# Performance work log

Measured on AMD Instinct MI355X. Metric: run time of the kernel, lower is better.

Reference implementation:

```python
import jax, jax.numpy as jnp
import numpy as np

B, S, D, V = 2, 2048, 4096, 32000

def setup_inputs() -> dict:
    key = jax.random.key(0)
    k1, k2, k3 = jax.random.split(key, 3)
    hidden_states = jax.random.normal(k1, (B, S, D), dtype=jnp.float32)
    W = jax.random.normal(k2, (V, D), dtype=jnp.float32) * 0.02  # lm_head weight [vocab, hidden]
    label_ids = jax.random.randint(k3, (B, S), 0, V, dtype=jnp.int64)
    return {"hidden_states": hidden_states, "W": W, "label_ids": label_ids}

def reference(hidden_states, W, label_ids):
    # lm_head: Linear(D, V, bias=False) -> logits [B, S, V], cast to fp32
    logits = jnp.einsum('bsd,vd->bsv', hidden_states, W).astype(jnp.float32)
    # shift: predict token t+1 from position t
    shift_logits = logits[:, :-1, :].reshape(-1, V)          # [B*(S-1), V]
    shift_labels = label_ids[:, 1:].reshape(-1)              # [B*(S-1)]
    logp = jax.nn.log_softmax(shift_logits, axis=-1)
    nll = -jnp.take_along_axis(logp, shift_labels[:, None], axis=1)[:, 0]
    loss = jnp.mean(nll)  # CrossEntropyLoss default reduction='mean'
    return loss, logits
```

## Files before the change

kernel.cpp:

```cpp
#include <hip/hip_runtime.h>
#include <hip/hip_bf16.h>

#define M_ 4096
#define N_ 32000
#define K_ 4096
#define S_ 2048
#define SM1 2047
#define NROWS 4094
#define NT_ 128

typedef __bf16 bf16x8 __attribute__((ext_vector_type(8)));
typedef float f32x4 __attribute__((ext_vector_type(4)));

#define GLDS16(g, l)                                                         \
  __builtin_amdgcn_global_load_lds(                                          \
      (__attribute__((address_space(1))) const void*)(g),                    \
      (__attribute__((address_space(3))) void*)(l), 16, 0, 0)
#define BAR() __builtin_amdgcn_s_barrier()
#define PRIO1() __builtin_amdgcn_s_setprio(1)
#define PRIO0() __builtin_amdgcn_s_setprio(0)
#define VMCNT(n) asm volatile("s_waitcnt vmcnt(" #n ")" ::: "memory")
#define LGKM0() asm volatile("s_waitcnt lgkmcnt(0)" ::: "memory")

__global__ __launch_bounds__(256) void cvt_f32_to_bf16(
    const float* __restrict__ in, bf16x8* __restrict__ out, long n8) {
  long i0 = (long)blockIdx.x * blockDim.x + threadIdx.x;
  long stride = (long)gridDim.x * blockDim.x;
  for (long i = i0; i < n8; i += stride) {
    const float4* p = reinterpret_cast<const float4*>(in) + i * 2;
    float4 a = p[0];
    float4 b = p[1];
    bf16x8 v;
    v[0] = (__bf16)a.x; v[1] = (__bf16)a.y; v[2] = (__bf16)a.z; v[3] = (__bf16)a.w;
    v[4] = (__bf16)b.x; v[5] = (__bf16)b.y; v[6] = (__bf16)b.z; v[7] = (__bf16)b.w;
    out[i] = v;
  }
}

__global__ __launch_bounds__(512, 2) void gemm256(
    const __bf16* __restrict__ A, const __bf16* __restrict__ B,
    float* __restrict__ C) {
  __shared__ __align__(1024) unsigned char smem[4][32768];

  const int tid = threadIdx.x;
  const int bid = blockIdx.x;
  const int wg = (bid & 7) * 250 + (bid >> 3);
  const int nblk = wg >> 4;
  const int mblk = wg & 15;
  const int m0 = mblk * 256;
  const int n0 = nblk * 256;

  const int w = tid >> 6;
  const int lane = tid & 63;
  const int wm = w >> 2;
  const int wn = w & 3;
  const int rl = lane & 15;
  const int cl = lane >> 4;

  f32x4 acc[8][4];
#pragma unroll
  for (int i = 0; i < 8; ++i)
#pragma unroll
    for (int j = 0; j < 4; ++j) acc[i][j] = (f32x4){0.f, 0.f, 0.f, 0.f};

  auto stA = [&](unsigned char* buf, int kt) {
#pragma unroll
    for (int j = 0; j < 2; ++j) {
      const int cd = j * 512 + tid;
      const int row = cd >> 2;
      const int c = (cd & 3) ^ (row & 3);
      GLDS16(A + (size_t)(m0 + row) * K_ + kt * 32 + c * 8, buf + cd * 16);
    }
  };
  auto stB = [&](unsigned char* buf, int kt) {
#pragma unroll
    for (int j = 0; j < 2; ++j) {
      const int cd = j * 512 + tid;
      const int row = cd >> 2;
      const int c = (cd & 3) ^ (row & 3);
      GLDS16(B + (size_t)(n0 + row) * K_ + kt * 32 + c * 8,
             buf + 16384 + cd * 16);
    }
  };
  auto ld = [&](const unsigned char* base, int row) -> bf16x8 {
    return *(const bf16x8*)(base + row * 64 + (((cl ^ row) & 3) << 4));
  };

  stA(smem[0], 0); stB(smem[0], 0);
  stA(smem[1], 1); stB(smem[1], 1);
  stA(smem[2], 2); stB(smem[2], 2);
  VMCNT(8);
  BAR();

  bf16x8 a[4], b[4];
  for (int s = 0; s < NT_; ++s) {
    const unsigned char* bufc = smem[s & 3];
    unsigned char* bufn = smem[(s + 3) & 3];
    const bool st = (s < NT_ - 3);

#pragma unroll
    for (int i = 0; i < 4; ++i) a[i] = ld(bufc, wm * 128 + i * 16 + rl);
#pragma unroll
    for (int j = 0; j < 4; ++j) b[j] = ld(bufc + 16384, wn * 64 + j * 16 + rl);
    if (st) stA(bufn, s + 3);
    BAR();
    LGKM0();
    PRIO1();
#pragma unroll
    for (int ii = 0; ii < 4; ++ii)
#pragma unroll
      for (int jj = 0; jj < 4; ++jj)
        acc[ii][jj] = __builtin_amdgcn_mfma_f32_16x16x32_bf16(
            a[ii], b[jj], acc[ii][jj], 0, 0, 0);
    PRIO0();
    BAR();

#pragma unroll
    for (int i = 0; i < 4; ++i) a[i] = ld(bufc, wm * 128 + 64 + i * 16 + rl);
    if (st) stB(bufn, s + 3);
    BAR();
    LGKM0();
    PRIO1();
#pragma unroll
    for (int ii = 0; ii < 4; ++ii)
#pragma unroll
      for (int jj = 0; jj < 4; ++jj)
        acc[4 + ii][jj] = __builtin_amdgcn_mfma_f32_16x16x32_bf16(
            a[ii], b[jj], acc[4 + ii][jj], 0, 0, 0);
    PRIO0();
    if (s < NT_ - 3) { VMCNT(8); }
    else if (s == NT_ - 3) { VMCNT(4); }
    else if (s == NT_ - 2) { VMCNT(0); }
    BAR();
  }

#pragma unroll
  for (int i = 0; i < 8; ++i)
#pragma unroll
    for (int j = 0; j < 4; ++j)
#pragma unroll
      for (int r = 0; r < 4; ++r) {
        const int grow = m0 + wm * 128 + i * 16 + cl * 4 + r;
        const int gcol = n0 + wn * 64 + j * 16 + rl;
        C[(size_t)grow * N_ + gcol] = acc[i][j][r];
      }
}

__global__ __launch_bounds__(256) void gemm_fb(const float* __restrict__ Ap,
                                               const float* __restrict__ Bp,
                                               float* __restrict__ Cp) {
  __shared__ __align__(1024) unsigned char smem[2][16384];
  const int tid = threadIdx.x;
  const int bid = blockIdx.x;
  const int swz = (bid & 7) * 1000 + (bid >> 3);
  const int nblk = swz >> 5;
  const int mblk = swz & 31;
  const int m0 = mblk * 128;
  const int n0 = nblk * 128;
  const int w = tid >> 6, lane = tid & 63;
  const int wm = w >> 1, wn = w & 1;
  const int rl = lane & 15, cl = lane >> 4;

  f32x4 acc[4][4];
#pragma unroll
  for (int i = 0; i < 4; ++i)
#pragma unroll
    for (int j = 0; j < 4; ++j) acc[i][j] = (f32x4){0.f, 0.f, 0.f, 0.f};

  auto stage = [&](int buf, int kt) {
    const int k0 = kt * 32;
#pragma unroll
    for (int j = 0; j < 2; ++j) {
      const int t = j * 256 + tid;
      const int row = t >> 2;
      const int c = t & 3;
      const int rp = row >> 1;
      const int pp = ((row & 1) * 4 + c) ^ (rp & 7);
      const int lb = rp * 128 + pp * 16;
      {
        const float4* g = (const float4*)(Ap + (size_t)(m0 + row) * K_ + k0 + c * 8);
        float4 x = g[0], y = g[1];
        bf16x8 v;
        v[0] = (__bf16)x.x; v[1] = (__bf16)x.y; v[2] = (__bf16)x.z; v[3] = (__bf16)x.w;
        v[4] = (__bf16)y.x; v[5] = (__bf16)y.y; v[6] = (__bf16)y.z; v[7] = (__bf16)y.w;
        *(bf16x8*)(&smem[buf][lb]) = v;
      }
      {
        const float4* g = (const float4*)(Bp + (size_t)(n0 + row) * K_ + k0 + c * 8);
        float4 x = g[0], y = g[1];
        bf16x8 v;
        v[0] = (__bf16)x.x; v[1] = (__bf16)x.y; v[2] = (__bf16)x.z; v[3] = (__bf16)x.w;
        v[4] = (__bf16)y.x; v[5] = (__bf16)y.y; v[6] = (__bf16)y.z; v[7] = (__bf16)y.w;
        *(bf16x8*)(&smem[buf][8192 + lb]) = v;
      }
    }
  };
  auto ldfrag = [&](const unsigned char* base, int row, int c) -> bf16x8 {
    const int rp = row >> 1;
    const int pp = ((row & 1) * 4 + c) ^ (rp & 7);
    return *(const bf16x8*)(base + rp * 128 + pp * 16);
  };
  auto compute = [&](int buf) {
    const unsigned char* bA = smem[buf];
    const unsigned char* bB = smem[buf] + 8192;
    bf16x8 af[4], bfv[4];
#pragma unroll
    for (int i = 0; i < 4; ++i) af[i] = ldfrag(bA, wm * 64 + i * 16 + rl, cl);
#pragma unroll
    for (int j = 0; j < 4; ++j) bfv[j] = ldfrag(bB, wn * 64 + j * 16 + rl, cl);
#pragma unroll
    for (int i = 0; i < 4; ++i)
#pragma unroll
      for (int j = 0; j < 4; ++j)
        acc[i][j] = __builtin_amdgcn_mfma_f32_16x16x32_bf16(af[i], bfv[j],
                                                            acc[i][j], 0, 0, 0);
  };

  stage(0, 0);
  __syncthreads();
  for (int kt = 0; kt < 128; kt += 2) {
    if (kt + 1 < 128) stage(1, kt + 1);
    compute(0);
    __syncthreads();
    if (kt + 2 < 128) stage(0, kt + 2);
    compute(1);
    __syncthreads();
  }
#pragma unroll
  for (int i = 0; i < 4; ++i)
#pragma unroll
    for (int j = 0; j < 4; ++j)
#pragma unroll
      for (int r = 0; r < 4; ++r) {
        const int grow = m0 + wm * 64 + i * 16 + cl * 4 + r;
        const int gcol = n0 + wn * 64 + j * 16 + rl;
        Cp[(size_t)grow * N_ + gcol] = acc[i][j][r];
      }
}

__global__ __launch_bounds__(256) void ce_rows(const float* __restrict__ logits,
                                               const int* __restrict__ labels,
                                               float* __restrict__ nll) {
  const int r = blockIdx.x;
  const int b = r / SM1;
  const int t = r - b * SM1;
  const float* row = logits + (size_t)(b * S_ + t) * N_;
  float m = -3.4e38f, s = 0.f;
  const float4* row4 = (const float4*)row;
  for (int i = threadIdx.x; i < 7936; i += 256) {
    float4 v = row4[i];
    float mx = fmaxf(fmaxf(v.x, v.y), fmaxf(v.z, v.w));
    if (mx > m) { s *= __expf(m - mx); m = mx; }
    s += __expf(v.x - m) + __expf(v.y - m) + __expf(v.z - m) + __expf(v.w - m);
  }
  {
    float v = row[31744 + threadIdx.x];
    if (v > m) { s *= __expf(m - v); m = v; }
    s += __expf(v - m);
  }
#pragma unroll
  for (int o = 32; o > 0; o >>= 1) {
    float m2 = __shfl_xor(m, o), s2 = __shfl_xor(s, o);
    float mn = fmaxf(m, m2);
    s = s * __expf(m - mn) + s2 * __expf(m2 - mn);
    m = mn;
  }
  __shared__ float rm[4], rs[4];
  if ((threadIdx.x & 63) == 0) { rm[threadIdx.x >> 6] = m; rs[threadIdx.x >> 6] = s; }
  __syncthreads();
  if (threadIdx.x == 0) {
    float M = fmaxf(fmaxf(rm[0], rm[1]), fmaxf(rm[2], rm[3]));
    float S = rs[0] * __expf(rm[0] - M) + rs[1] * __expf(rm[1] - M) +
              rs[2] * __expf(rm[2] - M) + rs[3] * __expf(rm[3] - M);
    nll[r] = M + __logf(S) - row[labels[b * S_ + t + 1]];
  }
}

__global__ __launch_bounds__(256) void reduce_loss(const float* __restrict__ nll,
                                                   float* __restrict__ out) {
  float s = 0.f;
  for (int i = threadIdx.x; i < NROWS; i += 256) s += nll[i];
#pragma unroll
  for (int o = 32; o > 0; o >>= 1) s += __shfl_xor(s, o);
  __shared__ float sb[4];
  if ((threadIdx.x & 63) == 0) sb[threadIdx.x >> 6] = s;
  __syncthreads();
  if (threadIdx.x == 0) out[0] = (sb[0] + sb[1] + sb[2] + sb[3]) / (float)NROWS;
}

extern "C" void kernel_launch(void* const* d_in, const int* in_sizes, int n_in,
                              void* d_out, int out_size, void* d_ws,
                              size_t ws_size, hipStream_t stream) {
  const float* h = (const float*)d_in[0];
  const float* Wf = (const float*)d_in[1];
  const int* labels = (const int*)d_in[2];
  float* out = (float*)d_out;
  float* logits = out + 1;

  const size_t abytes = (size_t)M_ * K_ * 2;
  const size_t bbytes = (size_t)N_ * K_ * 2;
  const size_t need = abytes + bbytes + (size_t)NROWS * sizeof(float);

  if (ws_size >= need) {
    unsigned char* base = (unsigned char*)d_ws;
    __bf16* hA = (__bf16*)base;
    __bf16* wB = (__bf16*)(base + abytes);
    float* nll = (float*)(base + abytes + bbytes);
    cvt_f32_to_bf16<<<2048, 256, 0, stream>>>(h, (bf16x8*)hA,
                                              (long)((size_t)M_ * K_ / 8));
    cvt_f32_to_bf16<<<4096, 256, 0, stream>>>(Wf, (bf16x8*)wB,
                                              (long)((size_t)N_ * K_ / 8));
    gemm256<<<2000, 512, 0, stream>>>(hA, wB, logits);
    ce_rows<<<4094, 256, 0, stream>>>(logits, labels, nll);
    reduce_loss<<<1, 256, 0, stream>>>(nll, out);
  } else {
    float* nll = (float*)d_ws;
    gemm_fb<<<8000, 256, 0, stream>>>(h, Wf, logits);
    ce_rows<<<4094, 256, 0, stream>>>(logits, labels, nll);
    reduce_loss<<<1, 256, 0, stream>>>(nll, out);
  }
}
```

Before: 1.351 ms.

## Restructure gemm256 main loop to BK=64 double-buffer with quartered MFMA phases

```diff
diff --git a/kernel.cpp b/kernel.cpp
--- a/kernel.cpp
+++ b/kernel.cpp
@@ -7,7 +7,7 @@
 #define S_ 2048
 #define SM1 2047
 #define NROWS 4094
-#define NT_ 128
+#define NT_ 64
 
 typedef __bf16 bf16x8 __attribute__((ext_vector_type(8)));
 typedef float f32x4 __attribute__((ext_vector_type(4)));
@@ -20,7 +20,6 @@
 #define PRIO1() __builtin_amdgcn_s_setprio(1)
 #define PRIO0() __builtin_amdgcn_s_setprio(0)
 #define VMCNT(n) asm volatile("s_waitcnt vmcnt(" #n ")" ::: "memory")
-#define LGKM0() asm volatile("s_waitcnt lgkmcnt(0)" ::: "memory")
 
 __global__ __launch_bounds__(256) void cvt_f32_to_bf16(
     const float* __restrict__ in, bf16x8* __restrict__ out, long n8) {
@@ -40,7 +39,7 @@
 __global__ __launch_bounds__(512, 2) void gemm256(
     const __bf16* __restrict__ A, const __bf16* __restrict__ B,
     float* __restrict__ C) {
-  __shared__ __align__(1024) unsigned char smem[4][32768];
+  __shared__ __align__(1024) unsigned char smem[2][65536];
 
   const int tid = threadIdx.x;
   const int bid = blockIdx.x;
@@ -56,6 +55,8 @@
   const int wn = w & 3;
   const int rl = lane & 15;
   const int cl = lane >> 4;
+  const int srow = tid >> 3;
+  const int scc = tid & 7;
 
   f32x4 acc[8][4];
 #pragma unroll
@@ -63,75 +64,132 @@
 #pragma unroll
     for (int j = 0; j < 4; ++j) acc[i][j] = (f32x4){0.f, 0.f, 0.f, 0.f};
 
-  auto stA = [&](unsigned char* buf, int kt) {
+  auto stA2 = [&](int nbuf, int kt, int q) {
 #pragma unroll
     for (int j = 0; j < 2; ++j) {
-      const int cd = j * 512 + tid;
-      const int row = cd >> 2;
-      const int c = (cd & 3) ^ (row & 3);
-      GLDS16(A + (size_t)(m0 + row) * K_ + kt * 32 + c * 8, buf + cd * 16);
+      const int r0 = q * 64 + j * 128;
+      const int row = r0 + srow;
+      const int c = scc ^ (row & 7);
+      GLDS16(A + (size_t)(m0 + row) * K_ + kt * 64 + c * 8,
+             &smem[nbuf][r0 * 128 + tid * 16]);
     }
   };
-  auto stB = [&](unsigned char* buf, int kt) {
+  auto stB2 = [&](int nbuf, int kt, int q) {
 #pragma unroll
     for (int j = 0; j < 2; ++j) {
-      const int cd = j * 512 + tid;
-      const int row = cd >> 2;
-      const int c = (cd & 3) ^ (row & 3);
-      GLDS16(B + (size_t)(n0 + row) * K_ + kt * 32 + c * 8,
-             buf + 16384 + cd * 16);
+      const int cg = j * 512 + tid;
+      const int rl_ = cg >> 3;
+      const int row = ((rl_ >> 5) << 6) + q * 32 + (rl_ & 31);
+      const int cc = cg & 7;
+      const int c = cc ^ (row & 7);
+      GLDS16(B + (size_t)(n0 + row) * K_ + kt * 64 + c * 8,
+             &smem[nbuf][32768 + row * 128 + cc * 16]);
     }
   };
-  auto ld = [&](const unsigned char* base, int row) -> bf16x8 {
-    return *(const bf16x8*)(base + row * 64 + (((cl ^ row) & 3) << 4));
-  };
-
-  stA(smem[0], 0); stB(smem[0], 0);
-  stA(smem[1], 1); stB(smem[1], 1);
-  stA(smem[2], 2); stB(smem[2], 2);
-  VMCNT(8);
+  auto ld = [&](const unsigned char* base, int row, int c) -> bf16x8 {
+    return *(const bf16x8*)(base + row * 128 + (((c ^ row) & 7) << 4));
+  };
+
+  stA2(0, 0, 0); stB2(0, 0, 0); stA2(0, 0, 1); stB2(0, 0, 1);
+  VMCNT(4);
   BAR();
 
-  bf16x8 a[4], b[4];
+  bf16x8 al[4][2], ah[4][2], b0r[2][2], b1r[2][2];
+#pragma unroll
+  for (int jj = 0; jj < 2; ++jj)
+#pragma unroll
+    for (int ks = 0; ks < 2; ++ks)
+      b0r[jj][ks] = ld(smem[0] + 32768, wn * 64 + jj * 16 + rl, ks * 4 + cl);
+#pragma unroll
+  for (int ii = 0; ii < 4; ++ii)
+#pragma unroll
+    for (int ks = 0; ks < 2; ++ks)
+      al[ii][ks] = ld(smem[0], wm * 128 + ii * 16 + rl, ks * 4 + cl);
+
   for (int s = 0; s < NT_; ++s) {
-    const unsigned char* bufc = smem[s & 3];
-    unsigned char* bufn = smem[(s + 3) & 3];
-    const bool st = (s < NT_ - 3);
-
-#pragma unroll
-    for (int i = 0; i < 4; ++i) a[i] = ld(bufc, wm * 128 + i * 16 + rl);
-#pragma unroll
-    for (int j = 0; j < 4; ++j) b[j] = ld(bufc + 16384, wn * 64 + j * 16 + rl);
-    if (st) stA(bufn, s + 3);
+    const int cur = s & 1;
+    const int nxt = cur ^ 1;
+    const unsigned char* bA = smem[cur];
+    const unsigned char* bB = smem[cur] + 32768;
+    const bool st = (s + 1 < NT_);
+
+    if (st) stA2(nxt, s + 1, 0);
+    PRIO1();
+#pragma unroll
+    for (int ii = 0; ii < 4; ++ii)
+#pragma unroll
+      for (int jj = 0; jj < 2; ++jj)
+#pragma unroll
+        for (int ks = 0; ks < 2; ++ks)
+          acc[ii][jj] = __builtin_amdgcn_mfma_f32_16x16x32_bf16(
+              al[ii][ks], b0r[jj][ks], acc[ii][jj], 0, 0, 0);
+    PRIO0();
+    if (st) { VMCNT(2); } else { VMCNT(0); }
     BAR();
-    LGKM0();
+
+    if (st) stB2(nxt, s + 1, 0);
+#pragma unroll
+    for (int jj = 0; jj < 2; ++jj)
+#pragma unroll
+      for (int ks = 0; ks < 2; ++ks)
+        b1r[jj][ks] = ld(bB, wn * 64 + 32 + jj * 16 + rl, ks * 4 + cl);
+#pragma unroll
+    for (int ii = 0; ii < 4; ++ii)
+#pragma unroll
+      for (int ks = 0; ks < 2; ++ks)
+        ah[ii][ks] = ld(bA, wm * 128 + 64 + ii * 16 + rl, ks * 4 + cl);
     PRIO1();
 #pragma unroll
     for (int ii = 0; ii < 4; ++ii)
 #pragma unroll
-      for (int jj = 0; jj < 4; ++jj)
-        acc[ii][jj] = __builtin_amdgcn_mfma_f32_16x16x32_bf16(
-            a[ii], b[jj], acc[ii][jj], 0, 0, 0);
+      for (int jj = 0; jj < 2; ++jj)
+#pragma unroll
+        for (int ks = 0; ks < 2; ++ks)
+          acc[ii][2 + jj] = __builtin_amdgcn_mfma_f32_16x16x32_bf16(
+              al[ii][ks], b1r[jj][ks], acc[ii][2 + jj], 0, 0, 0);
     PRIO0();
     BAR();
 
-#pragma unroll
-    for (int i = 0; i < 4; ++i) a[i] = ld(bufc, wm * 128 + 64 + i * 16 + rl);
-    if (st) stB(bufn, s + 3);
+    if (st) stA2(nxt, s + 1, 1);
+    PRIO1();
+#pragma unroll
+    for (int ii = 0; ii < 4; ++ii)
+#pragma unroll
+      for (int jj = 0; jj < 2; ++jj)
+#pragma unroll
+        for (int ks = 0; ks < 2; ++ks)
+          acc[4 + ii][jj] = __builtin_amdgcn_mfma_f32_16x16x32_bf16(
+              ah[ii][ks], b0r[jj][ks], acc[4 + ii][jj], 0, 0, 0);
+    PRIO0();
     BAR();
-    LGKM0();
+
+    if (st) stB2(nxt, s + 1, 1);
     PRIO1();
 #pragma unroll
     for (int ii = 0; ii < 4; ++ii)
 #pragma unroll
-      for (int jj = 0; jj < 4; ++jj)
-        acc[4 + ii][jj] = __builtin_amdgcn_mfma_f32_16x16x32_bf16(
-            a[ii], b[jj], acc[4 + ii][jj], 0, 0, 0);
+      for (int jj = 0; jj < 2; ++jj)
+#pragma unroll
+        for (int ks = 0; ks < 2; ++ks)
+          acc[4 + ii][2 + jj] = __builtin_amdgcn_mfma_f32_16x16x32_bf16(
+              ah[ii][ks], b1r[jj][ks], acc[4 + ii][2 + jj], 0, 0, 0);
     PRIO0();
-    if (s < NT_ - 3) { VMCNT(8); }
-    else if (s == NT_ - 3) { VMCNT(4); }
-    else if (s == NT_ - 2) { VMCNT(0); }
+    if (st) VMCNT(4);
     BAR();
+    if (st) {
+      const unsigned char* nA = smem[nxt];
+      const unsigned char* nB = smem[nxt] + 32768;
+#pragma unroll
+      for (int jj = 0; jj < 2; ++jj)
+#pragma unroll
+        for (int ks = 0; ks < 2; ++ks)
+          b0r[jj][ks] = ld(nB, wn * 64 + jj * 16 + rl, ks * 4 + cl);
+#pragma unroll
+      for (int ii = 0; ii < 4; ++ii)
+#pragma unroll
+        for (int ks = 0; ks < 2; ++ks)
+          al[ii][ks] = ld(nA, wm * 128 + ii * 16 + rl, ks * 4 + cl);
+    }
   }
 
 #pragma unroll
```

Result: faster. 1.244 ms (-8.0%).

## Fuse per-tile softmax partials into GEMM epilogue and simplify pipeline to double buffer

Applied to the files above, without the earlier changes.

```diff
diff --git a/kernel.cpp b/kernel.cpp
--- a/kernel.cpp
+++ b/kernel.cpp
@@ -8,6 +8,7 @@
 #define SM1 2047
 #define NROWS 4094
 #define NT_ 128
+#define NB_ 125
 
 typedef __bf16 bf16x8 __attribute__((ext_vector_type(8)));
 typedef float f32x4 __attribute__((ext_vector_type(4)));
@@ -20,7 +21,6 @@
 #define PRIO1() __builtin_amdgcn_s_setprio(1)
 #define PRIO0() __builtin_amdgcn_s_setprio(0)
 #define VMCNT(n) asm volatile("s_waitcnt vmcnt(" #n ")" ::: "memory")
-#define LGKM0() asm volatile("s_waitcnt lgkmcnt(0)" ::: "memory")
 
 __global__ __launch_bounds__(256) void cvt_f32_to_bf16(
     const float* __restrict__ in, bf16x8* __restrict__ out, long n8) {
@@ -39,8 +39,8 @@
 
 __global__ __launch_bounds__(512, 2) void gemm256(
     const __bf16* __restrict__ A, const __bf16* __restrict__ B,
-    float* __restrict__ C) {
-  __shared__ __align__(1024) unsigned char smem[4][32768];
+    float* __restrict__ C, float* __restrict__ pm, float* __restrict__ ps) {
+  __shared__ __align__(1024) unsigned char smem[2][32768];
 
   const int tid = threadIdx.x;
   const int bid = blockIdx.x;
@@ -67,8 +67,10 @@
 #pragma unroll
     for (int j = 0; j < 2; ++j) {
       const int cd = j * 512 + tid;
-      const int row = cd >> 2;
-      const int c = (cd & 3) ^ (row & 3);
+      const int p = cd >> 3;
+      const int pl = (cd & 7) ^ (p & 7);
+      const int row = p * 2 + (pl >> 2);
+      const int c = pl & 3;
       GLDS16(A + (size_t)(m0 + row) * K_ + kt * 32 + c * 8, buf + cd * 16);
     }
   };
@@ -76,62 +78,94 @@
 #pragma unroll
     for (int j = 0; j < 2; ++j) {
       const int cd = j * 512 + tid;
-      const int row = cd >> 2;
-      const int c = (cd & 3) ^ (row & 3);
+      const int p = cd >> 3;
+      const int pl = (cd & 7) ^ (p & 7);
+      const int row = p * 2 + (pl >> 2);
+      const int c = pl & 3;
       GLDS16(B + (size_t)(n0 + row) * K_ + kt * 32 + c * 8,
              buf + 16384 + cd * 16);
     }
   };
   auto ld = [&](const unsigned char* base, int row) -> bf16x8 {
-    return *(const bf16x8*)(base + row * 64 + (((cl ^ row) & 3) << 4));
+    const int p = row >> 1;
+    const int slot = (((row & 1) * 4 + cl) ^ (p & 7));
+    return *(const bf16x8*)(base + p * 128 + slot * 16);
   };
 
   stA(smem[0], 0); stB(smem[0], 0);
   stA(smem[1], 1); stB(smem[1], 1);
-  stA(smem[2], 2); stB(smem[2], 2);
-  VMCNT(8);
+  VMCNT(4);
   BAR();
 
-  bf16x8 a[4], b[4];
-  for (int s = 0; s < NT_; ++s) {
-    const unsigned char* bufc = smem[s & 3];
-    unsigned char* bufn = smem[(s + 3) & 3];
-    const bool st = (s < NT_ - 3);
-
-#pragma unroll
-    for (int i = 0; i < 4; ++i) a[i] = ld(bufc, wm * 128 + i * 16 + rl);
+  bf16x8 a[8], b[4];
+  for (int t = 0; t < NT_; ++t) {
+    unsigned char* bufc = smem[t & 1];
+
 #pragma unroll
     for (int j = 0; j < 4; ++j) b[j] = ld(bufc + 16384, wn * 64 + j * 16 + rl);
-    if (st) stA(bufn, s + 3);
+#pragma unroll
+    for (int i = 0; i < 8; ++i) a[i] = ld(bufc, wm * 128 + i * 16 + rl);
+
+    PRIO1();
+#pragma unroll
+    for (int i = 0; i < 8; ++i)
+#pragma unroll
+      for (int j = 0; j < 4; ++j)
+        acc[i][j] = __builtin_amdgcn_mfma_f32_16x16x32_bf16(a[i], b[j],
+                                                            acc[i][j], 0, 0, 0);
+    PRIO0();
+
     BAR();
-    LGKM0();
-    PRIO1();
-#pragma unroll
-    for (int ii = 0; ii < 4; ++ii)
-#pragma unroll
-      for (int jj = 0; jj < 4; ++jj)
-        acc[ii][jj] = __builtin_amdgcn_mfma_f32_16x16x32_bf16(
-            a[ii], b[jj], acc[ii][jj], 0, 0, 0);
-    PRIO0();
+
+    if (t + 2 < NT_) {
+      stA(bufc, t + 2);
+      stB(bufc, t + 2);
+      VMCNT(4);
+      BAR();
+    } else if (t + 1 < NT_) {
+      VMCNT(0);
+      BAR();
+    }
+  }
+
+  float* red = (float*)smem;
+  float* red2 = (float*)(smem[0] + 4096);
+  {
     BAR();
-
-#pragma unroll
-    for (int i = 0; i < 4; ++i) a[i] = ld(bufc, wm * 128 + 64 + i * 16 + rl);
-    if (st) stB(bufn, s + 3);
+#pragma unroll
+    for (int i = 0; i < 8; ++i)
+#pragma unroll
+      for (int r = 0; r < 4; ++r) {
+        float v = fmaxf(fmaxf(acc[i][0][r], acc[i][1][r]),
+                        fmaxf(acc[i][2][r], acc[i][3][r]));
+#pragma unroll
+        for (int o = 1; o < 16; o <<= 1) v = fmaxf(v, __shfl_xor(v, o));
+        if (rl == 0) red[wn * 256 + wm * 128 + i * 16 + cl * 4 + r] = v;
+      }
     BAR();
-    LGKM0();
-    PRIO1();
-#pragma unroll
-    for (int ii = 0; ii < 4; ++ii)
-#pragma unroll
-      for (int jj = 0; jj < 4; ++jj)
-        acc[4 + ii][jj] = __builtin_amdgcn_mfma_f32_16x16x32_bf16(
-            a[ii], b[jj], acc[4 + ii][jj], 0, 0, 0);
-    PRIO0();
-    if (s < NT_ - 3) { VMCNT(8); }
-    else if (s == NT_ - 3) { VMCNT(4); }
-    else if (s == NT_ - 2) { VMCNT(0); }
+#pragma unroll
+    for (int i = 0; i < 8; ++i)
+#pragma unroll
+      for (int r = 0; r < 4; ++r) {
+        const int row = wm * 128 + i * 16 + cl * 4 + r;
+        const float mx = fmaxf(fmaxf(red[row], red[256 + row]),
+                               fmaxf(red[512 + row], red[768 + row]));
+        float sv = __expf(acc[i][0][r] - mx) + __expf(acc[i][1][r] - mx) +
+                   __expf(acc[i][2][r] - mx) + __expf(acc[i][3][r] - mx);
+#pragma unroll
+        for (int o = 1; o < 16; o <<= 1) sv += __shfl_xor(sv, o);
+        if (rl == 0) red2[wn * 256 + row] = sv;
+      }
     BAR();
+    if (tid < 256) {
+      const int row = tid;
+      const float Mv = fmaxf(fmaxf(red[row], red[256 + row]),
+                             fmaxf(red[512 + row], red[768 + row]));
+      const float Sv = red2[row] + red2[256 + row] + red2[512 + row] +
+                       red2[768 + row];
+      pm[(size_t)(m0 + row) * NB_ + nblk] = Mv;
+      ps[(size_t)(m0 + row) * NB_ + nblk] = Sv;
+    }
   }
 
 #pragma unroll
@@ -144,6 +178,35 @@
         const int gcol = n0 + wn * 64 + j * 16 + rl;
         C[(size_t)grow * N_ + gcol] = acc[i][j][r];
       }
+}
+
+__global__ __launch_bounds__(64) void ce_combine(
+    const float* __restrict__ pm, const float* __restrict__ ps,
+    const float* __restrict__ logits, const int* __restrict__ labels,
+    float* __restrict__ nll) {
+  const int r = blockIdx.x;
+  const int b = r / SM1;
+  const int t = r - b * SM1;
+  const int m = b * S_ + t;
+  const int lane = threadIdx.x;
+  float M = -3.4e38f, Ssum = 0.f;
+  for (int j = lane; j < NB_; j += 64) {
+    const float mj = pm[(size_t)m * NB_ + j];
+    const float sj = ps[(size_t)m * NB_ + j];
+    if (mj > M) { Ssum *= __expf(M - mj); M = mj; }
+    Ssum += sj * __expf(mj - M);
+  }
+#pragma unroll
+  for (int o = 32; o > 0; o >>= 1) {
+    const float M2 = __shfl_xor(M, o), S2 = __shfl_xor(Ssum, o);
+    const float mn = fmaxf(M, M2);
+    Ssum = Ssum * __expf(M - mn) + S2 * __expf(M2 - mn);
+    M = mn;
+  }
+  if (lane == 0) {
+    const int lbl = labels[b * S_ + t + 1];
+    nll[r] = M + __logf(Ssum) - logits[(size_t)m * N_ + lbl];
+  }
 }
 
 __global__ __launch_bounds__(256) void gemm_fb(const float* __restrict__ Ap,
@@ -299,19 +362,22 @@
 
   const size_t abytes = (size_t)M_ * K_ * 2;
   const size_t bbytes = (size_t)N_ * K_ * 2;
-  const size_t need = abytes + bbytes + (size_t)NROWS * sizeof(float);
+  const size_t pbytes = (size_t)M_ * NB_ * 4;
+  const size_t need = abytes + bbytes + 2 * pbytes + (size_t)NROWS * 4;
 
   if (ws_size >= need) {
     unsigned char* base = (unsigned char*)d_ws;
     __bf16* hA = (__bf16*)base;
     __bf16* wB = (__bf16*)(base + abytes);
-    float* nll = (float*)(base + abytes + bbytes);
+    float* pm = (float*)(base + abytes + bbytes);
+    float* psum = (float*)(base + abytes + bbytes + pbytes);
+    float* nll = (float*)(base + abytes + bbytes + 2 * pbytes);
     cvt_f32_to_bf16<<<2048, 256, 0, stream>>>(h, (bf16x8*)hA,
                                               (long)((size_t)M_ * K_ / 8));
     cvt_f32_to_bf16<<<4096, 256, 0, stream>>>(Wf, (bf16x8*)wB,
                                               (long)((size_t)N_ * K_ / 8));
-    gemm256<<<2000, 512, 0, stream>>>(hA, wB, logits);
-    ce_rows<<<4094, 256, 0, stream>>>(logits, labels, nll);
+    gemm256<<<2000, 512, 0, stream>>>(hA, wB, logits, pm, psum);
+    ce_combine<<<NROWS, 64, 0, stream>>>(pm, psum, logits, labels, nll);
     reduce_loss<<<1, 256, 0, stream>>>(nll, out);
   } else {
     float* nll = (float*)d_ws;
```

Result: no change. 1.366 ms (+1.1%).
